# Performance work log

Hardware: AMD Instinct MI355X
Metric: run time of the kernel (lower is better)

Reference implementation:

```python
import jax, jax.numpy as jnp
import numpy as np

N = 50000
K = 32
C = 256  # hidden_dim

def setup_inputs() -> dict:
    key = jax.random.key(0)
    k1, k2, k3, k4 = jax.random.split(key, 4)
    feat = jax.random.normal(k1, (N, C), dtype=jnp.float32)
    coords = jax.random.normal(k2, (N, 3), dtype=jnp.float32)
    knn_idx = jax.random.randint(k3, (N, K), 0, N, dtype=jnp.int32)
    # Dense(hidden_dim) over concat([feat(C), agg(C), rel_mean(3), rel_std(3)]) -> in_dim = 2C + 6
    W = jax.random.normal(k4, (2 * C + 6, C), dtype=jnp.float32) * (1.0 / np.sqrt(2 * C + 6))
    b = jnp.zeros((C,), dtype=jnp.float32)
    return {"feat": feat, "coords": coords, "knn_idx": knn_idx, "W": W, "b": b}

def reference(feat, coords, knn_idx, W, b):
    # Neighbor feature aggregation: gather (N,K,C) then mean over K
    nbr_feat = feat[knn_idx]                      # (N, K, C)
    agg = jnp.mean(nbr_feat, axis=1)              # (N, C)
    # Relative coordinate statistics
    nbr_coords = coords[knn_idx]                  # (N, K, 3)
    rel = nbr_coords - coords[:, None, :]         # (N, K, 3)
    rel_mean = jnp.mean(rel, axis=1)              # (N, 3)
    rel_var = jnp.mean(jnp.square(rel), axis=1) - jnp.square(rel_mean)
    rel_std = jnp.sqrt(jnp.maximum(rel_var, 0.0))  # population std, like tf.math.reduce_std
    mix = jnp.concatenate([feat, agg, rel_mean, rel_std], axis=-1)  # (N, 2C+6)
    out = jax.nn.silu(mix @ W + b)                # (N, C)
    return out
```

## Files before the change

kernel.cpp:

```cpp
#include <hip/hip_runtime.h>
#include <math.h>


typedef __attribute__((ext_vector_type(8))) short short8;
typedef __attribute__((ext_vector_type(4))) float f32x4;
typedef __attribute__((ext_vector_type(2))) float f32x2;

constexpr int K = 32;
constexpr int C = 256;
constexpr int IN_DIM = 2 * C + 6;
constexpr int KP = 544;
constexpr int BM = 16;
constexpr int MIXS = 552;
constexpr int NT = 256;

__device__ __forceinline__ unsigned short f2bf(float f) {
  union { float f; unsigned u; } c; c.f = f;
  return (unsigned short)((c.u + 0x7fffu + ((c.u >> 16) & 1u)) >> 16);
}
__device__ __forceinline__ unsigned pack2(float lo, float hi) {
  return (unsigned)f2bf(lo) | ((unsigned)f2bf(hi) << 16);
}

__global__ __launch_bounds__(256) void prep_feat_q(const float* __restrict__ feat,
                                                   uint2* __restrict__ featq,
                                                   long total8) {
  long i = (long)blockIdx.x * 256 + threadIdx.x;
  if (i < total8) {
    const float4 v0 = reinterpret_cast<const float4*>(feat)[2 * i];
    const float4 v1 = reinterpret_cast<const float4*>(feat)[2 * i + 1];
    unsigned a = 0, b = 0;
    a = __builtin_amdgcn_cvt_pk_fp8_f32(v0.x, v0.y, a, false);
    a = __builtin_amdgcn_cvt_pk_fp8_f32(v0.z, v0.w, a, true);
    b = __builtin_amdgcn_cvt_pk_fp8_f32(v1.x, v1.y, b, false);
    b = __builtin_amdgcn_cvt_pk_fp8_f32(v1.z, v1.w, b, true);
    uint2 o; o.x = a; o.y = b;
    featq[i] = o;
  }
}

__global__ __launch_bounds__(256) void prep_w(const float* __restrict__ W,
                                              unsigned short* __restrict__ Wt) {
  int i = blockIdx.x * 256 + threadIdx.x;
  if (i < C * KP) {
    int nn = i / KP, k = i - nn * KP;
    float v = (k < IN_DIM) ? W[(size_t)k * C + nn] : 0.f;
    Wt[i] = f2bf(v);
  }
}

__global__ __launch_bounds__(NT, 4)
void gcl_main(const unsigned char* __restrict__ featq,
              const float* __restrict__ feat,
              const float* __restrict__ coords,
              const int*   __restrict__ knn,
              const unsigned short* __restrict__ Wt,
              const float* __restrict__ bias,
              float* __restrict__ out, int n)
{
  __shared__ unsigned short mix[BM][MIXS];
  __shared__ int knnLds[BM * K];

  const int t = threadIdx.x;
  const int row0 = blockIdx.x * BM;

  #pragma unroll
  for (int i = 0; i < (BM * K) / NT; ++i) {
    int e = t + i * NT;
    int r = e >> 5, k = e & 31;
    int g = row0 + r; if (g >= n) g = n - 1;
    knnLds[e] = knn[(size_t)g * K + k];
  }
  for (int e = t; e < BM * (KP - IN_DIM); e += NT) {
    int r = e / (KP - IN_DIM), c = e - r * (KP - IN_DIM);
    mix[r][IN_DIM + c] = 0;
  }
  __syncthreads();

  const int w    = t >> 6;
  const int lane = t & 63;
  const int cl   = lane & 15;
  const int rq   = lane >> 4;

  {
    const int r = (w << 2) + rq;
    int g = row0 + r; if (g >= n) g = n - 1;

    {
      const float4 s0 = *reinterpret_cast<const float4*>(feat + (size_t)g * C + cl * 16 + 0);
      const float4 s1 = *reinterpret_cast<const float4*>(feat + (size_t)g * C + cl * 16 + 4);
      const float4 s2 = *reinterpret_cast<const float4*>(feat + (size_t)g * C + cl * 16 + 8);
      const float4 s3 = *reinterpret_cast<const float4*>(feat + (size_t)g * C + cl * 16 + 12);
      uint4 o0, o1;
      o0.x = pack2(s0.x, s0.y); o0.y = pack2(s0.z, s0.w);
      o0.z = pack2(s1.x, s1.y); o0.w = pack2(s1.z, s1.w);
      o1.x = pack2(s2.x, s2.y); o1.y = pack2(s2.z, s2.w);
      o1.z = pack2(s3.x, s3.y); o1.w = pack2(s3.z, s3.w);
      *reinterpret_cast<uint4*>(&mix[r][cl * 16 + 0]) = o0;
      *reinterpret_cast<uint4*>(&mix[r][cl * 16 + 8]) = o1;
    }

    const int* ids = &knnLds[r * K];
    float a0=0,a1=0,a2=0,a3=0,a4=0,a5=0,a6=0,a7=0;
    float a8=0,a9=0,aA=0,aB=0,aC=0,aD=0,aE=0,aF=0;
    #pragma unroll 8
    for (int k = 0; k < K; ++k) {
      const uint4 v = *reinterpret_cast<const uint4*>(featq + (size_t)ids[k] * C + cl * 16);
      f32x2 d0 = __builtin_amdgcn_cvt_pk_f32_fp8(v.x, false);
      f32x2 d1 = __builtin_amdgcn_cvt_pk_f32_fp8(v.x, true);
      f32x2 d2 = __builtin_amdgcn_cvt_pk_f32_fp8(v.y, false);
      f32x2 d3 = __builtin_amdgcn_cvt_pk_f32_fp8(v.y, true);
      f32x2 d4 = __builtin_amdgcn_cvt_pk_f32_fp8(v.z, false);
      f32x2 d5 = __builtin_amdgcn_cvt_pk_f32_fp8(v.z, true);
      f32x2 d6 = __builtin_amdgcn_cvt_pk_f32_fp8(v.w, false);
      f32x2 d7 = __builtin_amdgcn_cvt_pk_f32_fp8(v.w, true);
      a0 += d0.x; a1 += d0.y; a2 += d1.x; a3 += d1.y;
      a4 += d2.x; a5 += d2.y; a6 += d3.x; a7 += d3.y;
      a8 += d4.x; a9 += d4.y; aA += d5.x; aB += d5.y;
      aC += d6.x; aD += d6.y; aE += d7.x; aF += d7.y;
    }
    const float s = 1.0f / 32.0f;
    uint4 o0, o1;
    o0.x = pack2(a0 * s, a1 * s); o0.y = pack2(a2 * s, a3 * s);
    o0.z = pack2(a4 * s, a5 * s); o0.w = pack2(a6 * s, a7 * s);
    o1.x = pack2(a8 * s, a9 * s); o1.y = pack2(aA * s, aB * s);
    o1.z = pack2(aC * s, aD * s); o1.w = pack2(aE * s, aF * s);
    *reinterpret_cast<uint4*>(&mix[r][C + cl * 16 + 0]) = o0;
    *reinterpret_cast<uint4*>(&mix[r][C + cl * 16 + 8]) = o1;
  }

  #pragma unroll
  for (int pass = 0; pass < 2; ++pass) {
    const int sr = (t >> 5) + pass * 8;
    const int sk = t & 31;
    const int id = knnLds[sr * K + sk];
    const float x = coords[(size_t)id * 3 + 0];
    const float y = coords[(size_t)id * 3 + 1];
    const float z = coords[(size_t)id * 3 + 2];
    float sx = x, sy = y, sz = z;
    float qx = x * x, qy = y * y, qz = z * z;
    #pragma unroll
    for (int m = 1; m < 32; m <<= 1) {
      sx += __shfl_xor(sx, m); sy += __shfl_xor(sy, m); sz += __shfl_xor(sz, m);
      qx += __shfl_xor(qx, m); qy += __shfl_xor(qy, m); qz += __shfl_xor(qz, m);
    }
    if (sk == 0) {
      int g = row0 + sr; if (g >= n) g = n - 1;
      const float inv = 1.0f / 32.0f;
      const float mx = sx * inv, my = sy * inv, mz = sz * inv;
      const float vx = qx * inv - mx * mx;
      const float vy = qy * inv - my * my;
      const float vz = qz * inv - mz * mz;
      mix[sr][2 * C + 0] = f2bf(mx - coords[(size_t)g * 3 + 0]);
      mix[sr][2 * C + 1] = f2bf(my - coords[(size_t)g * 3 + 1]);
      mix[sr][2 * C + 2] = f2bf(mz - coords[(size_t)g * 3 + 2]);
      mix[sr][2 * C + 3] = f2bf(sqrtf(fmaxf(vx, 0.f)));
      mix[sr][2 * C + 4] = f2bf(sqrtf(fmaxf(vy, 0.f)));
      mix[sr][2 * C + 5] = f2bf(sqrtf(fmaxf(vz, 0.f)));
    }
  }
  __syncthreads();

  const int n0  = w * 64;
  const int l15 = lane & 15;
  const int h   = lane >> 4;

  f32x4 acc[4];
  #pragma unroll
  for (int nt = 0; nt < 4; ++nt) acc[nt] = (f32x4){0.f, 0.f, 0.f, 0.f};

  const unsigned short* wbase = Wt + (size_t)(n0 + l15) * KP + 8 * h;

  #pragma unroll 1
  for (int s8 = 0; s8 < KP / 32; ++s8) {
    const int kb = s8 * 32;
    short8 A0 = *reinterpret_cast<const short8*>(&mix[l15][kb + 8 * h]);
    short8 B0 = *reinterpret_cast<const short8*>(wbase + 0 * 16 * KP + kb);
    short8 B1 = *reinterpret_cast<const short8*>(wbase + 1 * 16 * KP + kb);
    short8 B2 = *reinterpret_cast<const short8*>(wbase + 2 * 16 * KP + kb);
    short8 B3 = *reinterpret_cast<const short8*>(wbase + 3 * 16 * KP + kb);
    acc[0] = __builtin_amdgcn_mfma_f32_16x16x32_bf16(A0, B0, acc[0], 0, 0, 0);
    acc[1] = __builtin_amdgcn_mfma_f32_16x16x32_bf16(A0, B1, acc[1], 0, 0, 0);
    acc[2] = __builtin_amdgcn_mfma_f32_16x16x32_bf16(A0, B2, acc[2], 0, 0, 0);
    acc[3] = __builtin_amdgcn_mfma_f32_16x16x32_bf16(A0, B3, acc[3], 0, 0, 0);
  }

  #pragma unroll
  for (int nt = 0; nt < 4; ++nt) {
    const int col = n0 + nt * 16 + l15;
    const float bv = bias[col];
    f32x4 a = acc[nt];
    #pragma unroll
    for (int q = 0; q < 4; ++q) {
      const int grow = row0 + 4 * h + q;
      if (grow < n) {
        const float x = a[q] + bv;
        out[(size_t)grow * C + col] = x / (1.f + __expf(-x));
      }
    }
  }
}

constexpr int BMF = 32;
constexpr int MIX_STRIDE = 520;

#define FMA4(mcomp, wv)                                                        \
  a.x = fmaf((mcomp), (wv).x, a.x);                                            \
  a.y = fmaf((mcomp), (wv).y, a.y);                                            \
  a.z = fmaf((mcomp), (wv).z, a.z);                                            \
  a.w = fmaf((mcomp), (wv).w, a.w);

__global__ __launch_bounds__(256, 2)
void gcl_fused(const float* __restrict__ feat,
               const float* __restrict__ coords,
               const int*   __restrict__ knn,
               const float* __restrict__ W,
               const float* __restrict__ bias,
               float* __restrict__ out,
               int n)
{
  __shared__ float mix[BMF][MIX_STRIDE];
  __shared__ int   knnLds[BMF * K];

  const int t = threadIdx.x;
  const int row0 = blockIdx.x * BMF;

  #pragma unroll
  for (int i = 0; i < (BMF * K) / 256; ++i) {
    const int e = t + i * 256;
    const int r = e >> 5;
    const int k = e & (K - 1);
    int grow = row0 + r; if (grow >= n) grow = n - 1;
    knnLds[e] = knn[(size_t)grow * K + k];
  }
  __syncthreads();

  const int c4 = t & 63;
  const int rg = t >> 6;

  for (int ri = 0; ri < BMF / 4; ++ri) {
    const int r = rg * (BMF / 4) + ri;
    int grow = row0 + r; if (grow >= n) grow = n - 1;
    const int* ids = &knnLds[r * K];
    float sx = 0.f, sy = 0.f, sz = 0.f, sw = 0.f;
    #pragma unroll 8
    for (int k = 0; k < K; ++k) {
      const float4 f = *reinterpret_cast<const float4*>(feat + (size_t)ids[k] * C + c4 * 4);
      sx += f.x; sy += f.y; sz += f.z; sw += f.w;
    }
    const float4 self = *reinterpret_cast<const float4*>(feat + (size_t)grow * C + c4 * 4);
    float* mr = mix[r];
    *reinterpret_cast<float4*>(mr + c4 * 4) = self;
    const float inv = 1.0f / (float)K;
    float4 a; a.x = sx * inv; a.y = sy * inv; a.z = sz * inv; a.w = sw * inv;
    *reinterpret_cast<float4*>(mr + C + c4 * 4) = a;
  }

  if (t < BMF * 3) {
    const int r = t / 3;
    const int d = t - r * 3;
    int grow = row0 + r; if (grow >= n) grow = n - 1;
    const int* ids = &knnLds[r * K];
    float s = 0.f, ss = 0.f;
    #pragma unroll 8
    for (int k = 0; k < K; ++k) {
      const float v = coords[(size_t)ids[k] * 3 + d];
      s += v; ss += v * v;
    }
    const float inv = 1.0f / (float)K;
    const float m = s * inv;
    const float var = ss * inv - m * m;
    mix[r][2 * C + d]     = m - coords[(size_t)grow * 3 + d];
    mix[r][2 * C + 3 + d] = sqrtf(fmaxf(var, 0.f));
  }
  __syncthreads();

  const int c0 = (t & 63) * 4;
  const int rbase = rg * (BMF / 4);

  float4 acc[BMF / 4];
  {
    const float4 bv = *reinterpret_cast<const float4*>(bias + c0);
    #pragma unroll
    for (int ri = 0; ri < BMF / 4; ++ri) acc[ri] = bv;
  }

  for (int jb = 0; jb < 129; ++jb) {
    const int j = jb * 4;
    const float4 w0 = *reinterpret_cast<const float4*>(W + (size_t)(j + 0) * C + c0);
    const float4 w1 = *reinterpret_cast<const float4*>(W + (size_t)(j + 1) * C + c0);
    const float4 w2 = *reinterpret_cast<const float4*>(W + (size_t)(j + 2) * C + c0);
    const float4 w3 = *reinterpret_cast<const float4*>(W + (size_t)(j + 3) * C + c0);
    #pragma unroll
    for (int ri = 0; ri < BMF / 4; ++ri) {
      const float4 m4 = *reinterpret_cast<const float4*>(&mix[rbase + ri][j]);
      float4 a = acc[ri];
      FMA4(m4.x, w0)
      FMA4(m4.y, w1)
      FMA4(m4.z, w2)
      FMA4(m4.w, w3)
      acc[ri] = a;
    }
  }
  #pragma unroll
  for (int jt = IN_DIM - 2; jt < IN_DIM; ++jt) {
    const float4 wv = *reinterpret_cast<const float4*>(W + (size_t)jt * C + c0);
    #pragma unroll
    for (int ri = 0; ri < BMF / 4; ++ri) {
      const float m = mix[rbase + ri][jt];
      float4 a = acc[ri];
      FMA4(m, wv)
      acc[ri] = a;
    }
  }

  #pragma unroll
  for (int ri = 0; ri < BMF / 4; ++ri) {
    const int grow = row0 + rbase + ri;
    if (grow < n) {
      float4 a = acc[ri];
      a.x = a.x / (1.f + expf(-a.x));
      a.y = a.y / (1.f + expf(-a.y));
      a.z = a.z / (1.f + expf(-a.z));
      a.w = a.w / (1.f + expf(-a.w));
      *reinterpret_cast<float4*>(out + (size_t)grow * C + c0) = a;
    }
  }
}

extern "C" void kernel_launch(void* const* d_in, const int* in_sizes, int n_in,
                              void* d_out, int out_size, void* d_ws, size_t ws_size,
                              hipStream_t stream) {
  const float* feat   = (const float*)d_in[0];
  const float* coords = (const float*)d_in[1];
  const int*   knn    = (const int*)d_in[2];
  const float* W      = (const float*)d_in[3];
  const float* bias   = (const float*)d_in[4];
  float* out = (float*)d_out;

  const int n = in_sizes[0] / C;

  const size_t featq_bytes = (size_t)n * C;
  const size_t wt_bytes    = (size_t)C * KP * 2;

  if (ws_size >= featq_bytes + wt_bytes) {
    unsigned char* featq  = (unsigned char*)d_ws;
    unsigned short* Wt    = (unsigned short*)((char*)d_ws + featq_bytes);
    const long total8 = (long)n * C / 8;
    const int grid = (n + BM - 1) / BM;
    hipLaunchKernelGGL(prep_feat_q, dim3((unsigned)((total8 + 255) / 256)), dim3(256), 0, stream,
                       feat, (uint2*)featq, total8);
    hipLaunchKernelGGL(prep_w, dim3((C * KP + 255) / 256), dim3(256), 0, stream, W, Wt);
    hipLaunchKernelGGL(gcl_main, dim3(grid), dim3(NT), 0, stream,
                       featq, feat, coords, knn, Wt, bias, out, n);
  } else {
    const int gridf = (n + BMF - 1) / BMF;
    hipLaunchKernelGGL(gcl_fused, dim3(gridf), dim3(256), 0, stream,
                       feat, coords, knn, W, bias, out, n);
  }
}
```

Before: 133.8 us.

## Split neighbor gather into channel-sliced passes for cache locality

The fp8 feature table is re-laid out into four 64-channel slices, and the neighbor gather-mean runs as four separate kernel launches, one per slice. Each slice is about 3.2 MB, so it can stay cache-resident while the random gather runs. The aggregated mean is written to a bf16 workspace buffer and then loaded by a separate GEMM kernel. The cost is an extra round trip to global memory for the aggregate, more kernel launches, 64-byte random rows instead of 256-byte ones, and a larger workspace requirement that could send execution to the fallback path.

New measurement: 159.2 us. 1.19x slower.

```diff
diff --git a/kernel.cpp b/kernel.cpp
--- a/kernel.cpp
+++ b/kernel.cpp
@@ -10,9 +10,12 @@
 constexpr int C = 256;
 constexpr int IN_DIM = 2 * C + 6;
 constexpr int KP = 544;
+constexpr int NT = 256;
+constexpr int BMG = 64;
 constexpr int BM = 16;
 constexpr int MIXS = 552;
-constexpr int NT = 256;
+constexpr int SCH = 64;
+constexpr int NSLICE = 4;
 
 __device__ __forceinline__ unsigned short f2bf(float f) {
   union { float f; unsigned u; } c; c.f = f;
@@ -22,25 +25,26 @@
   return (unsigned)f2bf(lo) | ((unsigned)f2bf(hi) << 16);
 }
 
-__global__ __launch_bounds__(256) void prep_feat_q(const float* __restrict__ feat,
-                                                   uint2* __restrict__ featq,
-                                                   long total8) {
-  long i = (long)blockIdx.x * 256 + threadIdx.x;
-  if (i < total8) {
-    const float4 v0 = reinterpret_cast<const float4*>(feat)[2 * i];
-    const float4 v1 = reinterpret_cast<const float4*>(feat)[2 * i + 1];
+__global__ __launch_bounds__(256)
+void prep_tq(const float* __restrict__ feat, unsigned char* __restrict__ tS, int n) {
+  int i = blockIdx.x * 256 + threadIdx.x;
+  if (i < n * 32) {
+    const int r = i >> 5, c8 = i & 31;
+    const int ch0 = c8 * 8, s = ch0 >> 6, wi = ch0 & 63;
+    const float4 v0 = *reinterpret_cast<const float4*>(feat + (size_t)r * C + ch0);
+    const float4 v1 = *reinterpret_cast<const float4*>(feat + (size_t)r * C + ch0 + 4);
     unsigned a = 0, b = 0;
     a = __builtin_amdgcn_cvt_pk_fp8_f32(v0.x, v0.y, a, false);
     a = __builtin_amdgcn_cvt_pk_fp8_f32(v0.z, v0.w, a, true);
     b = __builtin_amdgcn_cvt_pk_fp8_f32(v1.x, v1.y, b, false);
     b = __builtin_amdgcn_cvt_pk_fp8_f32(v1.z, v1.w, b, true);
     uint2 o; o.x = a; o.y = b;
-    featq[i] = o;
-  }
-}
-
-__global__ __launch_bounds__(256) void prep_w(const float* __restrict__ W,
-                                              unsigned short* __restrict__ Wt) {
+    *reinterpret_cast<uint2*>(tS + (size_t)s * n * SCH + (size_t)r * SCH + wi) = o;
+  }
+}
+
+__global__ __launch_bounds__(256)
+void prep_w(const float* __restrict__ W, unsigned short* __restrict__ Wt) {
   int i = blockIdx.x * 256 + threadIdx.x;
   if (i < C * KP) {
     int nn = i / KP, k = i - nn * KP;
@@ -49,9 +53,66 @@
   }
 }
 
-__global__ __launch_bounds__(NT, 4)
-void gcl_main(const unsigned char* __restrict__ featq,
-              const float* __restrict__ feat,
+__global__ __launch_bounds__(NT)
+void gather_slice(const unsigned char* __restrict__ tS,
+                  const int* __restrict__ knn,
+                  unsigned short* __restrict__ agg,
+                  int n, int slice)
+{
+  __shared__ int knnLds[BMG * K];
+  const int t = threadIdx.x;
+  const int row0 = blockIdx.x * BMG;
+
+  #pragma unroll
+  for (int i = 0; i < (BMG * K) / NT; ++i) {
+    int e = t + i * NT;
+    int r = e >> 5, k = e & 31;
+    int g = row0 + r; if (g >= n) g = n - 1;
+    knnLds[e] = knn[(size_t)g * K + k];
+  }
+  __syncthreads();
+
+  const int row = t >> 2;
+  const int lp  = t & 3;
+  const unsigned char* base = tS + (size_t)slice * n * SCH + lp * 16;
+  const int* ids = &knnLds[row * K];
+
+  float a0=0,a1=0,a2=0,a3=0,a4=0,a5=0,a6=0,a7=0;
+  float a8=0,a9=0,aA=0,aB=0,aC=0,aD=0,aE=0,aF=0;
+  #pragma unroll 8
+  for (int k = 0; k < K; ++k) {
+    const uint4 v = *reinterpret_cast<const uint4*>(base + (size_t)ids[k] * SCH);
+    f32x2 d0 = __builtin_amdgcn_cvt_pk_f32_fp8(v.x, false);
+    f32x2 d1 = __builtin_amdgcn_cvt_pk_f32_fp8(v.x, true);
+    f32x2 d2 = __builtin_amdgcn_cvt_pk_f32_fp8(v.y, false);
+    f32x2 d3 = __builtin_amdgcn_cvt_pk_f32_fp8(v.y, true);
+    f32x2 d4 = __builtin_amdgcn_cvt_pk_f32_fp8(v.z, false);
+    f32x2 d5 = __builtin_amdgcn_cvt_pk_f32_fp8(v.z, true);
+    f32x2 d6 = __builtin_amdgcn_cvt_pk_f32_fp8(v.w, false);
+    f32x2 d7 = __builtin_amdgcn_cvt_pk_f32_fp8(v.w, true);
+    a0 += d0.x; a1 += d0.y; a2 += d1.x; a3 += d1.y;
+    a4 += d2.x; a5 += d2.y; a6 += d3.x; a7 += d3.y;
+    a8 += d4.x; a9 += d4.y; aA += d5.x; aB += d5.y;
+    aC += d6.x; aD += d6.y; aE += d7.x; aF += d7.y;
+  }
+
+  const int g = row0 + row;
+  if (g < n) {
+    const float s = 1.0f / 32.0f;
+    uint4 o0, o1;
+    o0.x = pack2(a0 * s, a1 * s); o0.y = pack2(a2 * s, a3 * s);
+    o0.z = pack2(a4 * s, a5 * s); o0.w = pack2(a6 * s, a7 * s);
+    o1.x = pack2(a8 * s, a9 * s); o1.y = pack2(aA * s, aB * s);
+    o1.z = pack2(aC * s, aD * s); o1.w = pack2(aE * s, aF * s);
+    unsigned short* dst = agg + (size_t)g * C + slice * SCH + lp * 16;
+    *reinterpret_cast<uint4*>(dst)     = o0;
+    *reinterpret_cast<uint4*>(dst + 8) = o1;
+  }
+}
+
+__global__ __launch_bounds__(NT)
+void gcl_gemm(const float* __restrict__ feat,
+              const unsigned short* __restrict__ agg,
               const float* __restrict__ coords,
               const int*   __restrict__ knn,
               const unsigned short* __restrict__ Wt,
@@ -85,48 +146,22 @@
   {
     const int r = (w << 2) + rq;
     int g = row0 + r; if (g >= n) g = n - 1;
-
-    {
-      const float4 s0 = *reinterpret_cast<const float4*>(feat + (size_t)g * C + cl * 16 + 0);
-      const float4 s1 = *reinterpret_cast<const float4*>(feat + (size_t)g * C + cl * 16 + 4);
-      const float4 s2 = *reinterpret_cast<const float4*>(feat + (size_t)g * C + cl * 16 + 8);
-      const float4 s3 = *reinterpret_cast<const float4*>(feat + (size_t)g * C + cl * 16 + 12);
-      uint4 o0, o1;
-      o0.x = pack2(s0.x, s0.y); o0.y = pack2(s0.z, s0.w);
-      o0.z = pack2(s1.x, s1.y); o0.w = pack2(s1.z, s1.w);
-      o1.x = pack2(s2.x, s2.y); o1.y = pack2(s2.z, s2.w);
-      o1.z = pack2(s3.x, s3.y); o1.w = pack2(s3.z, s3.w);
-      *reinterpret_cast<uint4*>(&mix[r][cl * 16 + 0]) = o0;
-      *reinterpret_cast<uint4*>(&mix[r][cl * 16 + 8]) = o1;
-    }
-
-    const int* ids = &knnLds[r * K];
-    float a0=0,a1=0,a2=0,a3=0,a4=0,a5=0,a6=0,a7=0;
-    float a8=0,a9=0,aA=0,aB=0,aC=0,aD=0,aE=0,aF=0;
-    #pragma unroll 8
-    for (int k = 0; k < K; ++k) {
-      const uint4 v = *reinterpret_cast<const uint4*>(featq + (size_t)ids[k] * C + cl * 16);
-      f32x2 d0 = __builtin_amdgcn_cvt_pk_f32_fp8(v.x, false);
-      f32x2 d1 = __builtin_amdgcn_cvt_pk_f32_fp8(v.x, true);
-      f32x2 d2 = __builtin_amdgcn_cvt_pk_f32_fp8(v.y, false);
-      f32x2 d3 = __builtin_amdgcn_cvt_pk_f32_fp8(v.y, true);
-      f32x2 d4 = __builtin_amdgcn_cvt_pk_f32_fp8(v.z, false);
-      f32x2 d5 = __builtin_amdgcn_cvt_pk_f32_fp8(v.z, true);
-      f32x2 d6 = __builtin_amdgcn_cvt_pk_f32_fp8(v.w, false);
-      f32x2 d7 = __builtin_amdgcn_cvt_pk_f32_fp8(v.w, true);
-      a0 += d0.x; a1 += d0.y; a2 += d1.x; a3 += d1.y;
-      a4 += d2.x; a5 += d2.y; a6 += d3.x; a7 += d3.y;
-      a8 += d4.x; a9 += d4.y; aA += d5.x; aB += d5.y;
-      aC += d6.x; aD += d6.y; aE += d7.x; aF += d7.y;
-    }
-    const float s = 1.0f / 32.0f;
+    const float4 s0 = *reinterpret_cast<const float4*>(feat + (size_t)g * C + cl * 16 + 0);
+    const float4 s1 = *reinterpret_cast<const float4*>(feat + (size_t)g * C + cl * 16 + 4);
+    const float4 s2 = *reinterpret_cast<const float4*>(feat + (size_t)g * C + cl * 16 + 8);
+    const float4 s3 = *reinterpret_cast<const float4*>(feat + (size_t)g * C + cl * 16 + 12);
     uint4 o0, o1;
-    o0.x = pack2(a0 * s, a1 * s); o0.y = pack2(a2 * s, a3 * s);
-    o0.z = pack2(a4 * s, a5 * s); o0.w = pack2(a6 * s, a7 * s);
-    o1.x = pack2(a8 * s, a9 * s); o1.y = pack2(aA * s, aB * s);
-    o1.z = pack2(aC * s, aD * s); o1.w = pack2(aE * s, aF * s);
-    *reinterpret_cast<uint4*>(&mix[r][C + cl * 16 + 0]) = o0;
-    *reinterpret_cast<uint4*>(&mix[r][C + cl * 16 + 8]) = o1;
+    o0.x = pack2(s0.x, s0.y); o0.y = pack2(s0.z, s0.w);
+    o0.z = pack2(s1.x, s1.y); o0.w = pack2(s1.z, s1.w);
+    o1.x = pack2(s2.x, s2.y); o1.y = pack2(s2.z, s2.w);
+    o1.z = pack2(s3.x, s3.y); o1.w = pack2(s3.z, s3.w);
+    *reinterpret_cast<uint4*>(&mix[r][cl * 16 + 0]) = o0;
+    *reinterpret_cast<uint4*>(&mix[r][cl * 16 + 8]) = o1;
+
+    const uint4 g0 = *reinterpret_cast<const uint4*>(agg + (size_t)g * C + cl * 16 + 0);
+    const uint4 g1 = *reinterpret_cast<const uint4*>(agg + (size_t)g * C + cl * 16 + 8);
+    *reinterpret_cast<uint4*>(&mix[r][C + cl * 16 + 0]) = g0;
+    *reinterpret_cast<uint4*>(&mix[r][C + cl * 16 + 8]) = g1;
   }
 
   #pragma unroll
@@ -340,19 +375,29 @@
 
   const int n = in_sizes[0] / C;
 
-  const size_t featq_bytes = (size_t)n * C;
-  const size_t wt_bytes    = (size_t)C * KP * 2;
-
-  if (ws_size >= featq_bytes + wt_bytes) {
-    unsigned char* featq  = (unsigned char*)d_ws;
-    unsigned short* Wt    = (unsigned short*)((char*)d_ws + featq_bytes);
-    const long total8 = (long)n * C / 8;
-    const int grid = (n + BM - 1) / BM;
-    hipLaunchKernelGGL(prep_feat_q, dim3((unsigned)((total8 + 255) / 256)), dim3(256), 0, stream,
-                       feat, (uint2*)featq, total8);
+  const size_t tS_bytes  = (size_t)n * C;
+  const size_t wt_bytes  = (size_t)C * KP * 2;
+  const size_t agg_bytes = (size_t)n * C * 2;
+  const size_t need = tS_bytes + wt_bytes + agg_bytes;
+
+  if (ws_size >= need) {
+    unsigned char*  tS  = (unsigned char*)d_ws;
+    unsigned short* Wt  = (unsigned short*)((char*)d_ws + tS_bytes);
+    unsigned short* agg = (unsigned short*)((char*)d_ws + tS_bytes + wt_bytes);
+
+    hipLaunchKernelGGL(prep_tq, dim3((n * 32 + 255) / 256), dim3(256), 0, stream,
+                       feat, tS, n);
     hipLaunchKernelGGL(prep_w, dim3((C * KP + 255) / 256), dim3(256), 0, stream, W, Wt);
-    hipLaunchKernelGGL(gcl_main, dim3(grid), dim3(NT), 0, stream,
-                       featq, feat, coords, knn, Wt, bias, out, n);
+
+    const int gridG = (n + BMG - 1) / BMG;
+    for (int s = 0; s < NSLICE; ++s) {
+      hipLaunchKernelGGL(gather_slice, dim3(gridG), dim3(NT), 0, stream,
+                         tS, knn, agg, n, s);
+    }
+
+    const int gridM = (n + BM - 1) / BM;
+    hipLaunchKernelGGL(gcl_gemm, dim3(gridM), dim3(NT), 0, stream,
+                       feat, agg, coords, knn, Wt, bias, out, n);
   } else {
     const int gridf = (n + BMF - 1) / BMF;
     hipLaunchKernelGGL(gcl_fused, dim3(gridf), dim3(256), 0, stream,
```

## Double rows per block, prefetch MFMA operands, fold mean scale into W

Applied to the files above, without the earlier changes.

Raises the row tile from 16 to 32 so each wave computes two 16-row MFMA tiles and reuses every weight fragment loaded from global memory twice, halving weight traffic per row. The K loop is software-pipelined so the next step's A and B fragments load while the current MFMAs run. The 1/32 mean scale moves into the preprocessed weights, bf16 packing switches to the hardware v_cvt_pk_bf16_f32 instruction, and the SiLU divide becomes a reciprocal multiply. The larger tile doubles LDS use and raises register pressure, which may lower occupancy, and the reciprocal is slightly less precise.

Result: faster. 124.9 us (-6.6%).

```diff
diff --git a/kernel.cpp b/kernel.cpp
--- a/kernel.cpp
+++ b/kernel.cpp
@@ -10,7 +10,7 @@
 constexpr int C = 256;
 constexpr int IN_DIM = 2 * C + 6;
 constexpr int KP = 544;
-constexpr int BM = 16;
+constexpr int BM = 32;
 constexpr int MIXS = 552;
 constexpr int NT = 256;
 
@@ -18,8 +18,10 @@
   union { float f; unsigned u; } c; c.f = f;
   return (unsigned short)((c.u + 0x7fffu + ((c.u >> 16) & 1u)) >> 16);
 }
-__device__ __forceinline__ unsigned pack2(float lo, float hi) {
-  return (unsigned)f2bf(lo) | ((unsigned)f2bf(hi) << 16);
+__device__ __forceinline__ unsigned cvtpk(float lo, float hi) {
+  unsigned r;
+  asm("v_cvt_pk_bf16_f32 %0, %1, %2" : "=v"(r) : "v"(lo), "v"(hi));
+  return r;
 }
 
 __global__ __launch_bounds__(256) void prep_feat_q(const float* __restrict__ feat,
@@ -45,6 +47,7 @@
   if (i < C * KP) {
     int nn = i / KP, k = i - nn * KP;
     float v = (k < IN_DIM) ? W[(size_t)k * C + nn] : 0.f;
+    if (k >= C && k < 2 * C) v *= (1.0f / 32.0f);
     Wt[i] = f2bf(v);
   }
 }
@@ -82,8 +85,9 @@
   const int cl   = lane & 15;
   const int rq   = lane >> 4;
 
-  {
-    const int r = (w << 2) + rq;
+  #pragma unroll
+  for (int p = 0; p < 2; ++p) {
+    const int r = (w << 3) + (p << 2) + rq;
     int g = row0 + r; if (g >= n) g = n - 1;
 
     {
@@ -92,10 +96,10 @@
       const float4 s2 = *reinterpret_cast<const float4*>(feat + (size_t)g * C + cl * 16 + 8);
       const float4 s3 = *reinterpret_cast<const float4*>(feat + (size_t)g * C + cl * 16 + 12);
       uint4 o0, o1;
-      o0.x = pack2(s0.x, s0.y); o0.y = pack2(s0.z, s0.w);
-      o0.z = pack2(s1.x, s1.y); o0.w = pack2(s1.z, s1.w);
-      o1.x = pack2(s2.x, s2.y); o1.y = pack2(s2.z, s2.w);
-      o1.z = pack2(s3.x, s3.y); o1.w = pack2(s3.z, s3.w);
+      o0.x = cvtpk(s0.x, s0.y); o0.y = cvtpk(s0.z, s0.w);
+      o0.z = cvtpk(s1.x, s1.y); o0.w = cvtpk(s1.z, s1.w);
+      o1.x = cvtpk(s2.x, s2.y); o1.y = cvtpk(s2.z, s2.w);
+      o1.z = cvtpk(s3.x, s3.y); o1.w = cvtpk(s3.z, s3.w);
       *reinterpret_cast<uint4*>(&mix[r][cl * 16 + 0]) = o0;
       *reinterpret_cast<uint4*>(&mix[r][cl * 16 + 8]) = o1;
     }
@@ -119,18 +123,17 @@
       a8 += d4.x; a9 += d4.y; aA += d5.x; aB += d5.y;
       aC += d6.x; aD += d6.y; aE += d7.x; aF += d7.y;
     }
-    const float s = 1.0f / 32.0f;
     uint4 o0, o1;
-    o0.x = pack2(a0 * s, a1 * s); o0.y = pack2(a2 * s, a3 * s);
-    o0.z = pack2(a4 * s, a5 * s); o0.w = pack2(a6 * s, a7 * s);
-    o1.x = pack2(a8 * s, a9 * s); o1.y = pack2(aA * s, aB * s);
-    o1.z = pack2(aC * s, aD * s); o1.w = pack2(aE * s, aF * s);
+    o0.x = cvtpk(a0, a1); o0.y = cvtpk(a2, a3);
+    o0.z = cvtpk(a4, a5); o0.w = cvtpk(a6, a7);
+    o1.x = cvtpk(a8, a9); o1.y = cvtpk(aA, aB);
+    o1.z = cvtpk(aC, aD); o1.w = cvtpk(aE, aF);
     *reinterpret_cast<uint4*>(&mix[r][C + cl * 16 + 0]) = o0;
     *reinterpret_cast<uint4*>(&mix[r][C + cl * 16 + 8]) = o1;
   }
 
   #pragma unroll
-  for (int pass = 0; pass < 2; ++pass) {
+  for (int pass = 0; pass < 4; ++pass) {
     const int sr = (t >> 5) + pass * 8;
     const int sk = t & 31;
     const int id = knnLds[sr * K + sk];
@@ -165,37 +168,60 @@
   const int l15 = lane & 15;
   const int h   = lane >> 4;
 
-  f32x4 acc[4];
-  #pragma unroll
-  for (int nt = 0; nt < 4; ++nt) acc[nt] = (f32x4){0.f, 0.f, 0.f, 0.f};
-
-  const unsigned short* wbase = Wt + (size_t)(n0 + l15) * KP + 8 * h;
+  f32x4 acc[2][4];
+  #pragma unroll
+  for (int mt = 0; mt < 2; ++mt)
+    #pragma unroll
+    for (int nt = 0; nt < 4; ++nt)
+      acc[mt][nt] = (f32x4){0.f, 0.f, 0.f, 0.f};
+
+  const unsigned short* wb = Wt + (size_t)(n0 + l15) * KP + 8 * h;
+
+  short8 B0 = *reinterpret_cast<const short8*>(wb + 0 * 16 * KP);
+  short8 B1 = *reinterpret_cast<const short8*>(wb + 1 * 16 * KP);
+  short8 B2 = *reinterpret_cast<const short8*>(wb + 2 * 16 * KP);
+  short8 B3 = *reinterpret_cast<const short8*>(wb + 3 * 16 * KP);
+  short8 A0 = *reinterpret_cast<const short8*>(&mix[l15][8 * h]);
+  short8 A1 = *reinterpret_cast<const short8*>(&mix[16 + l15][8 * h]);
 
   #pragma unroll 1
   for (int s8 = 0; s8 < KP / 32; ++s8) {
-    const int kb = s8 * 32;
-    short8 A0 = *reinterpret_cast<const short8*>(&mix[l15][kb + 8 * h]);
-    short8 B0 = *reinterpret_cast<const short8*>(wbase + 0 * 16 * KP + kb);
-    short8 B1 = *reinterpret_cast<const short8*>(wbase + 1 * 16 * KP + kb);
-    short8 B2 = *reinterpret_cast<const short8*>(wbase + 2 * 16 * KP + kb);
-    short8 B3 = *reinterpret_cast<const short8*>(wbase + 3 * 16 * KP + kb);
-    acc[0] = __builtin_amdgcn_mfma_f32_16x16x32_bf16(A0, B0, acc[0], 0, 0, 0);
-    acc[1] = __builtin_amdgcn_mfma_f32_16x16x32_bf16(A0, B1, acc[1], 0, 0, 0);
-    acc[2] = __builtin_amdgcn_mfma_f32_16x16x32_bf16(A0, B2, acc[2], 0, 0, 0);
-    acc[3] = __builtin_amdgcn_mfma_f32_16x16x32_bf16(A0, B3, acc[3], 0, 0, 0);
-  }
-
-  #pragma unroll
-  for (int nt = 0; nt < 4; ++nt) {
-    const int col = n0 + nt * 16 + l15;
-    const float bv = bias[col];
-    f32x4 a = acc[nt];
-    #pragma unroll
-    for (int q = 0; q < 4; ++q) {
-      const int grow = row0 + 4 * h + q;
-      if (grow < n) {
-        const float x = a[q] + bv;
-        out[(size_t)grow * C + col] = x / (1.f + __expf(-x));
+    const int kb  = s8 * 32;
+    const int kbn = (kb + 32 <= KP - 32) ? kb + 32 : KP - 32;
+    short8 nB0 = *reinterpret_cast<const short8*>(wb + 0 * 16 * KP + kbn);
+    short8 nB1 = *reinterpret_cast<const short8*>(wb + 1 * 16 * KP + kbn);
+    short8 nB2 = *reinterpret_cast<const short8*>(wb + 2 * 16 * KP + kbn);
+    short8 nB3 = *reinterpret_cast<const short8*>(wb + 3 * 16 * KP + kbn);
+    short8 nA0 = *reinterpret_cast<const short8*>(&mix[l15][kbn + 8 * h]);
+    short8 nA1 = *reinterpret_cast<const short8*>(&mix[16 + l15][kbn + 8 * h]);
+
+    acc[0][0] = __builtin_amdgcn_mfma_f32_16x16x32_bf16(A0, B0, acc[0][0], 0, 0, 0);
+    acc[1][0] = __builtin_amdgcn_mfma_f32_16x16x32_bf16(A1, B0, acc[1][0], 0, 0, 0);
+    acc[0][1] = __builtin_amdgcn_mfma_f32_16x16x32_bf16(A0, B1, acc[0][1], 0, 0, 0);
+    acc[1][1] = __builtin_amdgcn_mfma_f32_16x16x32_bf16(A1, B1, acc[1][1], 0, 0, 0);
+    acc[0][2] = __builtin_amdgcn_mfma_f32_16x16x32_bf16(A0, B2, acc[0][2], 0, 0, 0);
+    acc[1][2] = __builtin_amdgcn_mfma_f32_16x16x32_bf16(A1, B2, acc[1][2], 0, 0, 0);
+    acc[0][3] = __builtin_amdgcn_mfma_f32_16x16x32_bf16(A0, B3, acc[0][3], 0, 0, 0);
+    acc[1][3] = __builtin_amdgcn_mfma_f32_16x16x32_bf16(A1, B3, acc[1][3], 0, 0, 0);
+
+    B0 = nB0; B1 = nB1; B2 = nB2; B3 = nB3;
+    A0 = nA0; A1 = nA1;
+  }
+
+  #pragma unroll
+  for (int mt = 0; mt < 2; ++mt) {
+    #pragma unroll
+    for (int nt = 0; nt < 4; ++nt) {
+      const int col = n0 + nt * 16 + l15;
+      const float bv = bias[col];
+      f32x4 a = acc[mt][nt];
+      #pragma unroll
+      for (int q = 0; q < 4; ++q) {
+        const int grow = row0 + mt * 16 + 4 * h + q;
+        if (grow < n) {
+          const float x = a[q] + bv;
+          out[(size_t)grow * C + col] = x * __builtin_amdgcn_rcpf(1.f + __expf(-x));
+        }
       }
     }
   }
```
